# Kernel optimization log

Hardware: AMD Instinct MI355X
Metric: run time of the kernel (lower is better)

## Reference

```python
import jax, jax.numpy as jnp
import numpy as np

N_NODES = 50000
N_EDGES = 800000
IN_C, HID, OUT_C = 128, 128, 16
N_GRAPHS = 128


def setup_inputs() -> dict:
    key = jax.random.key(0)
    ks = jax.random.split(key, 8)
    x = jax.random.normal(ks[0], (N_NODES, IN_C), dtype=jnp.float32)
    edge_index = jax.random.randint(ks[1], (2, N_EDGES), 0, N_NODES, dtype=jnp.int64)
    batch = jnp.sort(jax.random.randint(ks[2], (N_NODES,), 0, N_GRAPHS, dtype=jnp.int64))
    s1 = 1.0 / np.sqrt(IN_C)
    s2 = 1.0 / np.sqrt(HID)
    W1 = jax.random.normal(ks[3], (IN_C, HID), dtype=jnp.float32) * s1
    b1 = jnp.zeros((HID,), dtype=jnp.float32)
    W2 = jax.random.normal(ks[4], (HID, HID), dtype=jnp.float32) * s2
    b2 = jnp.zeros((HID,), dtype=jnp.float32)
    Wfc = jax.random.normal(ks[5], (HID, OUT_C), dtype=jnp.float32) * s2
    bfc = jnp.zeros((OUT_C,), dtype=jnp.float32)
    return {"x": x, "edge_index": edge_index, "batch": batch,
            "W1": W1, "b1": b1, "W2": W2, "b2": b2, "Wfc": Wfc, "bfc": bfc}


def _gcn_conv(x, W, b, src, dst, deg_inv_sqrt, n_nodes):
    # linear transform first (PyG order), then normalized sparse aggregation
    h = x @ W  # [N, H]
    norm = deg_inv_sqrt[src] * deg_inv_sqrt[dst]  # [E+N] (self-loops appended)
    msgs = h[src] * norm[:, None]  # [E+N, H] dominant gather
    agg = jax.ops.segment_sum(msgs, dst, num_segments=n_nodes)
    return agg + b


def reference(x, edge_index, batch, W1, b1, W2, b2, Wfc, bfc):
    n = x.shape[0]
    loops = jnp.arange(n, dtype=edge_index.dtype)
    src = jnp.concatenate([edge_index[0], loops])
    dst = jnp.concatenate([edge_index[1], loops])
    # symmetric normalization with self-loops: deg computed on dst
    deg = jax.ops.segment_sum(jnp.ones_like(src, dtype=x.dtype), dst, num_segments=n)
    deg_inv_sqrt = jnp.where(deg > 0, jax.lax.rsqrt(jnp.maximum(deg, 1.0)), 0.0)

    h = jax.nn.relu(_gcn_conv(x, W1, b1, src, dst, deg_inv_sqrt, n))
    h = jax.nn.relu(_gcn_conv(h, W2, b2, src, dst, deg_inv_sqrt, n))

    # global mean pool over graph ids
    sums = jax.ops.segment_sum(h, batch, num_segments=N_GRAPHS)
    counts = jax.ops.segment_sum(jnp.ones((n,), dtype=h.dtype), batch, num_segments=N_GRAPHS)
    pooled = sums / jnp.maximum(counts, 1.0)[:, None]  # [G, H]

    logits = pooled @ Wfc + bfc  # [G, OUT_C]
    return jax.nn.log_softmax(logits, axis=1)
```

## Files before the change

### kernel.cpp

```cpp
#include <hip/hip_runtime.h>

#define N_NODES  50000
#define N_EDGES  800000
#define HID      128
#define OUT_C    16
#define N_GRAPHS 128
#define MAXDEG   64
#define NSLICE   6250
#define EPB      8192
#define FILLB    784
#define GEMMB    782
#define PREPW    64
#define AGB      3125
#define PAD      136

typedef __attribute__((ext_vector_type(8))) short bf16x8;
typedef __attribute__((ext_vector_type(4))) float f32x4;
typedef __attribute__((ext_vector_type(8))) unsigned short us8;
typedef __attribute__((ext_vector_type(4))) unsigned short us4;

__device__ __forceinline__ unsigned short f2bf(float f) {
  unsigned u = __float_as_uint(f);
  u += 0x7fffu + ((u >> 16) & 1u);
  return (unsigned short)(u >> 16);
}

__device__ __forceinline__ void gemm_compute_store(
    unsigned short* sA, const float* __restrict__ W,
    unsigned short* __restrict__ T, int base) {
  const int tid = threadIdx.x;
  const int lane = tid & 63;
  const int w = tid >> 6;
  const int l15 = lane & 15;
  const int quad = lane >> 4;
  __syncthreads();

  f32x4 acc[4][2];
#pragma unroll
  for (int nt = 0; nt < 4; ++nt)
#pragma unroll
    for (int c = 0; c < 2; ++c) acc[nt][c] = (f32x4)(0.f);

  const int ct0 = w * 2;
  const int ncol = ct0 * 16 + l15;
#pragma unroll
  for (int ks = 0; ks < 4; ++ks) {
    const int koff = ks * 32 + quad * 8;
    bf16x8 a[4], bfr[2];
#pragma unroll
    for (int c = 0; c < 2; ++c) {
      const float* wp = W + (size_t)koff * HID + ncol + c * 16;
#pragma unroll
      for (int j = 0; j < 8; ++j) bfr[c][j] = (short)f2bf(wp[(size_t)j * HID]);
    }
#pragma unroll
    for (int nt = 0; nt < 4; ++nt)
      a[nt] = *(const bf16x8*)(sA + (nt * 16 + l15) * PAD + koff);
#pragma unroll
    for (int nt = 0; nt < 4; ++nt)
#pragma unroll
      for (int c = 0; c < 2; ++c)
        acc[nt][c] = __builtin_amdgcn_mfma_f32_16x16x32_bf16(a[nt], bfr[c], acc[nt][c], 0, 0, 0);
  }
  __syncthreads();

#pragma unroll
  for (int nt = 0; nt < 4; ++nt)
#pragma unroll
    for (int c = 0; c < 2; ++c)
#pragma unroll
      for (int r = 0; r < 4; ++r)
        sA[(nt * 16 + quad * 4 + r) * PAD + (ct0 + c) * 16 + l15] = f2bf(acc[nt][c][r]);
  __syncthreads();
#pragma unroll
  for (int i = 0; i < 4; ++i) {
    int idx = tid + i * 256;
    int nrow = idx >> 4;
    int col = (idx & 15) * 8;
    int node = base + nrow;
    if (node < N_NODES)
      *(us8*)(T + (size_t)node * HID + col) = *(const us8*)(sA + nrow * PAD + col);
  }
}

__device__ __forceinline__ void stage_a_f32(unsigned short* sA,
                                            const float* __restrict__ H, int base) {
#pragma unroll
  for (int i = 0; i < 8; ++i) {
    int idx = threadIdx.x + i * 256;
    int nrow = idx >> 5;
    int c4 = (idx & 31) * 4;
    float4 v = make_float4(0.f, 0.f, 0.f, 0.f);
    int node = base + nrow;
    if (node < N_NODES) v = *(const float4*)(H + (size_t)node * HID + c4);
    us4 b;
    b.x = f2bf(v.x); b.y = f2bf(v.y); b.z = f2bf(v.z); b.w = f2bf(v.w);
    *(us4*)(sA + nrow * PAD + c4) = b;
  }
}

__global__ __launch_bounds__(256) void mega_kernel(
    const int* __restrict__ src, const int* __restrict__ dst,
    int* __restrict__ deg, unsigned short* __restrict__ ell,
    const int* __restrict__ batch, int* __restrict__ start,
    const float* __restrict__ x, const float* __restrict__ W1,
    unsigned short* __restrict__ T,
    const float* __restrict__ W2, unsigned short* __restrict__ wt2) {
  __shared__ unsigned short sA[64 * PAD];
  int b = blockIdx.x;
  if (b < FILLB) {
    const int slice = b & 7;
    const int e0 = (b >> 3) * EPB;
    const int e1 = min(e0 + EPB, N_EDGES);
    const unsigned lo = slice * NSLICE;
    for (int e = e0 + threadIdx.x; e < e1; e += 256) {
      int d = __builtin_nontemporal_load(dst + e);
      if ((unsigned)(d - lo) < (unsigned)NSLICE) {
        int p = atomicAdd(&deg[d], 1);
        if (p < MAXDEG) ell[(d << 6) + p] = (unsigned short)src[e];
      }
    }
  } else if (b == FILLB) {
    int t = threadIdx.x;
    if (t <= N_GRAPHS) {
      int lo = 0, hi = N_NODES;
      while (lo < hi) {
        int mid = (lo + hi) >> 1;
        if (batch[mid] < t) lo = mid + 1; else hi = mid;
      }
      start[t] = lo;
    }
  } else if (b < FILLB + 1 + GEMMB) {
    const int base = (b - FILLB - 1) * 64;
    stage_a_f32(sA, x, base);
    gemm_compute_store(sA, W1, T, base);
  } else {
    int idx = (b - FILLB - 1 - GEMMB) * 256 + threadIdx.x;
    int k = idx >> 7, n = idx & 127;
    wt2[n * HID + k] = f2bf(W2[k * HID + n]);
  }
}

__device__ __forceinline__ void agg_node(
    int node, int lane, const unsigned int* __restrict__ Tb,
    const unsigned short* __restrict__ ell, const int* __restrict__ deg,
    float bx, float by, float& ox, float& oy) {
  int dn = deg[node];
  float dd = rsqrtf((float)dn + 1.0f);
  unsigned sv = Tb[(size_t)node * 64 + lane];
  float wself = dd * dd;
  float ax = __int_as_float(sv << 16) * wself;
  float ay = __int_as_float(sv & 0xffff0000u) * wself;
  int m = min(dn, MAXDEG);
  int s0 = node << 6;
  int sidx = 0; float wv = 0.f;
  if (lane < m) {
    sidx = (int)ell[s0 + lane];
    wv = rsqrtf((float)deg[sidx] + 1.0f) * dd;
  }
  int j = 0;
  for (; j + 8 <= m; j += 8) {
#pragma unroll
    for (int q = 0; q < 8; ++q) {
      int s = __builtin_amdgcn_readlane(sidx, j + q);
      float w = __int_as_float(__builtin_amdgcn_readlane(__float_as_int(wv), j + q));
      unsigned t = Tb[(size_t)s * 64 + lane];
      ax += w * __int_as_float(t << 16);
      ay += w * __int_as_float(t & 0xffff0000u);
    }
  }
  for (; j < m; ++j) {
    int s = __builtin_amdgcn_readlane(sidx, j);
    float w = __int_as_float(__builtin_amdgcn_readlane(__float_as_int(wv), j));
    unsigned t = Tb[(size_t)s * 64 + lane];
    ax += w * __int_as_float(t << 16);
    ay += w * __int_as_float(t & 0xffff0000u);
  }
  ox = fmaxf(ax + bx, 0.f);
  oy = fmaxf(ay + by, 0.f);
}

__global__ __launch_bounds__(1024) void agg_gemm_kernel(
    const unsigned int* __restrict__ Tb, const unsigned short* __restrict__ ell,
    const int* __restrict__ deg, const float* __restrict__ bias,
    const unsigned short* __restrict__ wt2, unsigned short* __restrict__ T2) {
  __shared__ unsigned short sA[16 * PAD];
  const int tid = threadIdx.x;
  const int lane = tid & 63;
  const int w = tid >> 6;
  const int l15 = lane & 15;
  const int quad = lane >> 4;
  const int base = blockIdx.x * 16;

  {
    float2 b = ((const float2*)bias)[lane];
    float ox, oy;
    agg_node(base + w, lane, Tb, ell, deg, b.x, b.y, ox, oy);
    *(unsigned*)(sA + w * PAD + lane * 2) =
        (unsigned)f2bf(ox) | ((unsigned)f2bf(oy) << 16);
  }
  __syncthreads();

  f32x4 acc = (f32x4)(0.f);
  if (w < 8) {
    const unsigned short* wrow = wt2 + (size_t)(w * 16 + l15) * HID;
#pragma unroll
    for (int ks = 0; ks < 4; ++ks) {
      const int koff = ks * 32 + quad * 8;
      bf16x8 a = *(const bf16x8*)(sA + l15 * PAD + koff);
      bf16x8 bfr = *(const bf16x8*)(wrow + koff);
      acc = __builtin_amdgcn_mfma_f32_16x16x32_bf16(a, bfr, acc, 0, 0, 0);
    }
  }
  __syncthreads();
  if (w < 8) {
#pragma unroll
    for (int r = 0; r < 4; ++r)
      sA[(quad * 4 + r) * PAD + w * 16 + l15] = f2bf(acc[r]);
  }
  __syncthreads();
  if (tid < 256) {
    int nrow = tid >> 4;
    int col = (tid & 15) * 8;
    *(us8*)(T2 + (size_t)(base + nrow) * HID + col) = *(const us8*)(sA + nrow * PAD + col);
  }
}

__global__ __launch_bounds__(256) void aggregate_kernel(
    const unsigned int* __restrict__ Tb, const unsigned short* __restrict__ ell,
    const int* __restrict__ deg, const float* __restrict__ bias,
    unsigned int* __restrict__ Hb) {
  int node = (blockIdx.x * blockDim.x + threadIdx.x) >> 6;
  int lane = threadIdx.x & 63;
  if (node >= N_NODES) return;
  float2 b = ((const float2*)bias)[lane];
  float ox, oy;
  agg_node(node, lane, Tb, ell, deg, b.x, b.y, ox, oy);
  Hb[(size_t)node * 64 + lane] =
      (unsigned)f2bf(ox) | ((unsigned)f2bf(oy) << 16);
}

__global__ __launch_bounds__(256) void pool_partial_kernel(
    const unsigned int* __restrict__ Hb, const int* __restrict__ start,
    float* __restrict__ pooled) {
  __shared__ float2 red[4][64];
  int g = blockIdx.x >> 2;
  int chunk = blockIdx.x & 3;
  int n0 = start[g], n1 = start[g + 1];
  int lane = threadIdx.x & 63, w = threadIdx.x >> 6;
  float ax = 0.f, ay = 0.f;
  for (int n = n0 + chunk * 4 + w; n < n1; n += 16) {
    unsigned h = Hb[(size_t)n * 64 + lane];
    ax += __int_as_float(h << 16);
    ay += __int_as_float(h & 0xffff0000u);
  }
  red[w][lane] = make_float2(ax, ay);
  __syncthreads();
  if (threadIdx.x < 64) {
    float2 a = red[0][lane], b = red[1][lane], c = red[2][lane], d = red[3][lane];
    atomicAdd(&pooled[g * HID + lane * 2],     a.x + b.x + c.x + d.x);
    atomicAdd(&pooled[g * HID + lane * 2 + 1], a.y + b.y + c.y + d.y);
  }
}

__global__ __launch_bounds__(64) void head_kernel(
    const float* __restrict__ pooled, const int* __restrict__ start,
    const float* __restrict__ Wfc, const float* __restrict__ bfc,
    float* __restrict__ out) {
  int g = blockIdx.x;
  int lane = threadIdx.x;
  int o = lane & 15;
  float inv = 1.0f / fmaxf((float)(start[g + 1] - start[g]), 1.0f);
  float part = 0.f;
  for (int k = (lane >> 4); k < HID; k += 4)
    part += pooled[g * HID + k] * inv * Wfc[k * OUT_C + o];
  part += __shfl_xor(part, 16);
  part += __shfl_xor(part, 32);
  float logit = part + bfc[o];
  float m = logit;
#pragma unroll
  for (int d = 8; d >= 1; d >>= 1) m = fmaxf(m, __shfl_xor(m, d, 16));
  float e = __expf(logit - m);
  float s = e;
#pragma unroll
  for (int d = 8; d >= 1; d >>= 1) s += __shfl_xor(s, d, 16);
  float r = logit - m - __logf(s);
  if (lane < 16) out[g * OUT_C + o] = r;
}

extern "C" void kernel_launch(void* const* d_in, const int* in_sizes, int n_in,
                              void* d_out, int out_size, void* d_ws, size_t ws_size,
                              hipStream_t stream) {
  const float* x    = (const float*)d_in[0];
  const int*   ei   = (const int*)d_in[1];
  const int*   batch= (const int*)d_in[2];
  const float* W1   = (const float*)d_in[3];
  const float* b1   = (const float*)d_in[4];
  const float* W2   = (const float*)d_in[5];
  const float* b2   = (const float*)d_in[6];
  const float* Wfc  = (const float*)d_in[7];
  const float* bfc  = (const float*)d_in[8];
  float* out = (float*)d_out;
  const int* src = ei;
  const int* dst = ei + N_EDGES;

  char* p = (char*)d_ws;
  auto alloc = [&](size_t bytes) { char* r = p; p += (bytes + 255) & ~255ull; return r; };
  int*   degI   = (int*)alloc((size_t)N_NODES * 4);
  int*   start  = (int*)alloc((N_GRAPHS + 1) * 4);
  float* pooled = (float*)alloc((size_t)N_GRAPHS * HID * 4);
  unsigned short* wt2 = (unsigned short*)alloc((size_t)HID * HID * 2);
  unsigned short* ell = (unsigned short*)alloc((size_t)N_NODES * MAXDEG * 2);
  unsigned short* T   = (unsigned short*)alloc((size_t)N_NODES * HID * 2);
  unsigned short* T2  = (unsigned short*)alloc((size_t)N_NODES * HID * 2);
  unsigned short* Hb  = (unsigned short*)alloc((size_t)N_NODES * HID * 2);

  hipMemsetAsync(degI, 0, (size_t)N_NODES * 4, stream);
  hipMemsetAsync(pooled, 0, (size_t)N_GRAPHS * HID * 4, stream);

  int agg_blocks = (N_NODES * 64 + 255) / 256;

  mega_kernel<<<FILLB + 1 + GEMMB + PREPW, 256, 0, stream>>>(
      src, dst, degI, ell, batch, start, x, W1, T, W2, wt2);
  agg_gemm_kernel<<<AGB, 1024, 0, stream>>>((const unsigned int*)T, ell, degI,
                                            b1, wt2, T2);
  aggregate_kernel<<<agg_blocks, 256, 0, stream>>>((const unsigned int*)T2, ell, degI, b2,
                                                   (unsigned int*)Hb);
  pool_partial_kernel<<<N_GRAPHS * 4, 256, 0, stream>>>((const unsigned int*)Hb, start,
                                                        pooled);
  head_kernel<<<N_GRAPHS, 64, 0, stream>>>(pooled, start, Wfc, bfc, out);
}
```

Baseline: 250.2 us.

## Split each wavefront into four edge groups with 16-byte row gathers

Node aggregation changes from one lane per feature pair, walking neighbors one after another via readlane, to four quarter-wave groups. Each group handles every fourth neighbor, and each lane loads 8 bf16 features with one 16-byte load. Partial sums are combined with xor shuffles, then bias and relu are applied. The aim is to put more independent gathers in flight and use wider loads, cutting the serialized per-edge latency chain. In exchange it adds shuffle reductions and more registers, and only a quarter of the lanes write the output.

```diff
diff --git a/kernel.cpp b/kernel.cpp
--- a/kernel.cpp
+++ b/kernel.cpp
@@ -141,47 +141,69 @@
   }
 }
 
-__device__ __forceinline__ void agg_node(
-    int node, int lane, const unsigned int* __restrict__ Tb,
+__device__ __forceinline__ void agg_node8(
+    int node, int lane, const us8* __restrict__ T8,
     const unsigned short* __restrict__ ell, const int* __restrict__ deg,
-    float bx, float by, float& ox, float& oy) {
+    const float* __restrict__ bias, float* acc) {
+  const int l15 = lane & 15;
+  const int quad = lane >> 4;
   int dn = deg[node];
   float dd = rsqrtf((float)dn + 1.0f);
-  unsigned sv = Tb[(size_t)node * 64 + lane];
-  float wself = dd * dd;
-  float ax = __int_as_float(sv << 16) * wself;
-  float ay = __int_as_float(sv & 0xffff0000u) * wself;
   int m = min(dn, MAXDEG);
-  int s0 = node << 6;
-  int sidx = 0; float wv = 0.f;
-  if (lane < m) {
-    sidx = (int)ell[s0 + lane];
-    wv = rsqrtf((float)deg[sidx] + 1.0f) * dd;
-  }
-  int j = 0;
-  for (; j + 8 <= m; j += 8) {
-#pragma unroll
-    for (int q = 0; q < 8; ++q) {
-      int s = __builtin_amdgcn_readlane(sidx, j + q);
-      float w = __int_as_float(__builtin_amdgcn_readlane(__float_as_int(wv), j + q));
-      unsigned t = Tb[(size_t)s * 64 + lane];
-      ax += w * __int_as_float(t << 16);
-      ay += w * __int_as_float(t & 0xffff0000u);
-    }
-  }
-  for (; j < m; ++j) {
-    int s = __builtin_amdgcn_readlane(sidx, j);
-    float w = __int_as_float(__builtin_amdgcn_readlane(__float_as_int(wv), j));
-    unsigned t = Tb[(size_t)s * 64 + lane];
-    ax += w * __int_as_float(t << 16);
-    ay += w * __int_as_float(t & 0xffff0000u);
-  }
-  ox = fmaxf(ax + bx, 0.f);
-  oy = fmaxf(ay + by, 0.f);
+  if (quad == 0) {
+    us8 sv = T8[(size_t)node * 16 + l15];
+    float ws = dd * dd;
+#pragma unroll
+    for (int c = 0; c < 8; ++c)
+      acc[c] = ws * __int_as_float((unsigned)sv[c] << 16);
+  } else {
+#pragma unroll
+    for (int c = 0; c < 8; ++c) acc[c] = 0.f;
+  }
+  int mr = (m + 3) >> 2;
+  for (int jg = 0; jg < mr; jg += 8) {
+    int lim = min(8, mr - jg);
+    int s[8];
+#pragma unroll
+    for (int q = 0; q < 8; ++q)
+      if (q < lim) {
+        int e = (jg + q) * 4 + quad;
+        s[q] = (e < m) ? (int)ell[(node << 6) + e] : -1;
+      }
+    us8 t[8]; float w[8];
+#pragma unroll
+    for (int q = 0; q < 8; ++q)
+      if (q < lim) {
+        int sq = (s[q] < 0) ? 0 : s[q];
+        t[q] = T8[(size_t)sq * 16 + l15];
+        w[q] = (s[q] < 0) ? 0.f : rsqrtf((float)deg[sq] + 1.0f) * dd;
+      }
+#pragma unroll
+    for (int q = 0; q < 8; ++q)
+      if (q < lim)
+#pragma unroll
+        for (int c = 0; c < 8; ++c)
+          acc[c] += w[q] * __int_as_float((unsigned)t[q][c] << 16);
+  }
+#pragma unroll
+  for (int c = 0; c < 8; ++c) {
+    acc[c] += __shfl_xor(acc[c], 16);
+    acc[c] += __shfl_xor(acc[c], 32);
+  }
+  const float4 b0 = *(const float4*)(bias + l15 * 8);
+  const float4 b1 = *(const float4*)(bias + l15 * 8 + 4);
+  acc[0] = fmaxf(acc[0] + b0.x, 0.f);
+  acc[1] = fmaxf(acc[1] + b0.y, 0.f);
+  acc[2] = fmaxf(acc[2] + b0.z, 0.f);
+  acc[3] = fmaxf(acc[3] + b0.w, 0.f);
+  acc[4] = fmaxf(acc[4] + b1.x, 0.f);
+  acc[5] = fmaxf(acc[5] + b1.y, 0.f);
+  acc[6] = fmaxf(acc[6] + b1.z, 0.f);
+  acc[7] = fmaxf(acc[7] + b1.w, 0.f);
 }
 
 __global__ __launch_bounds__(1024) void agg_gemm_kernel(
-    const unsigned int* __restrict__ Tb, const unsigned short* __restrict__ ell,
+    const us8* __restrict__ T8, const unsigned short* __restrict__ ell,
     const int* __restrict__ deg, const float* __restrict__ bias,
     const unsigned short* __restrict__ wt2, unsigned short* __restrict__ T2) {
   __shared__ unsigned short sA[16 * PAD];
@@ -193,11 +215,14 @@
   const int base = blockIdx.x * 16;
 
   {
-    float2 b = ((const float2*)bias)[lane];
-    float ox, oy;
-    agg_node(base + w, lane, Tb, ell, deg, b.x, b.y, ox, oy);
-    *(unsigned*)(sA + w * PAD + lane * 2) =
-        (unsigned)f2bf(ox) | ((unsigned)f2bf(oy) << 16);
+    float acc[8];
+    agg_node8(base + w, lane, T8, ell, deg, bias, acc);
+    if (quad == 0) {
+      us8 o;
+#pragma unroll
+      for (int c = 0; c < 8; ++c) o[c] = f2bf(acc[c]);
+      *(us8*)(sA + w * PAD + l15 * 8) = o;
+    }
   }
   __syncthreads();
 
@@ -227,17 +252,20 @@
 }
 
 __global__ __launch_bounds__(256) void aggregate_kernel(
-    const unsigned int* __restrict__ Tb, const unsigned short* __restrict__ ell,
+    const us8* __restrict__ T8, const unsigned short* __restrict__ ell,
     const int* __restrict__ deg, const float* __restrict__ bias,
-    unsigned int* __restrict__ Hb) {
+    unsigned short* __restrict__ Hb) {
   int node = (blockIdx.x * blockDim.x + threadIdx.x) >> 6;
   int lane = threadIdx.x & 63;
   if (node >= N_NODES) return;
-  float2 b = ((const float2*)bias)[lane];
-  float ox, oy;
-  agg_node(node, lane, Tb, ell, deg, b.x, b.y, ox, oy);
-  Hb[(size_t)node * 64 + lane] =
-      (unsigned)f2bf(ox) | ((unsigned)f2bf(oy) << 16);
+  float acc[8];
+  agg_node8(node, lane, T8, ell, deg, bias, acc);
+  if ((lane >> 4) == 0) {
+    us8 o;
+#pragma unroll
+    for (int c = 0; c < 8; ++c) o[c] = f2bf(acc[c]);
+    *(us8*)(Hb + (size_t)node * HID + (lane & 15) * 8) = o;
+  }
 }
 
 __global__ __launch_bounds__(256) void pool_partial_kernel(
@@ -322,10 +350,9 @@
 
   mega_kernel<<<FILLB + 1 + GEMMB + PREPW, 256, 0, stream>>>(
       src, dst, degI, ell, batch, start, x, W1, T, W2, wt2);
-  agg_gemm_kernel<<<AGB, 1024, 0, stream>>>((const unsigned int*)T, ell, degI,
+  agg_gemm_kernel<<<AGB, 1024, 0, stream>>>((const us8*)T, ell, degI,
                                             b1, wt2, T2);
-  aggregate_kernel<<<agg_blocks, 256, 0, stream>>>((const unsigned int*)T2, ell, degI, b2,
-                                                   (unsigned int*)Hb);
+  aggregate_kernel<<<agg_blocks, 256, 0, stream>>>((const us8*)T2, ell, degI, b2, Hb);
   pool_partial_kernel<<<N_GRAPHS * 4, 256, 0, stream>>>((const unsigned int*)Hb, start,
                                                         pooled);
   head_kernel<<<N_GRAPHS, 64, 0, stream>>>(pooled, start, Wfc, bfc, out);
```

New measurement: 299.8 us. 19.8% more time.
